# Kernel tuning notes

Hardware: AMD Instinct MI355X
Metric: run time of the kernel (lower is better)

## Reference

```python
import jax, jax.numpy as jnp
import numpy as np

B, F_DIM, H, W = 4, 256, 32, 32
DIM, DEPTH, HEADS, MLP_DIM = 768, 8, 12, 3072
DIM_HEAD = DIM // HEADS
SCALE = DIM_HEAD ** -0.5
LN_EPS = 1e-5


def sine_pos_embed(h, w, num_pos_feats):
    # PositionEmbeddingSine with normalize=True, scale=2*pi, temperature=10000
    scale = 2.0 * np.pi
    eps = 1e-6
    y = jnp.arange(1, h + 1, dtype=jnp.float32) / (h + eps) * scale  # [h]
    x = jnp.arange(1, w + 1, dtype=jnp.float32) / (w + eps) * scale  # [w]
    i = jnp.arange(num_pos_feats, dtype=jnp.float32)
    dim_t = 10000.0 ** (2.0 * jnp.floor(i / 2.0) / num_pos_feats)  # [F]

    def interleave(p):  # p: [..., F] -> sin of even dims, cos of odd dims, interleaved
        return jnp.stack([jnp.sin(p[..., 0::2]), jnp.cos(p[..., 1::2])], axis=-1).reshape(p.shape[:-1] + (-1,))

    pos_y = interleave(y[:, None] / dim_t)  # [h, F]
    pos_x = interleave(x[:, None] / dim_t)  # [w, F]
    pos = jnp.concatenate([
        jnp.broadcast_to(pos_y[:, None, :], (h, w, num_pos_feats)),
        jnp.broadcast_to(pos_x[None, :, :], (h, w, num_pos_feats)),
    ], axis=-1)  # [h, w, 2F]
    return pos.reshape(h * w, 2 * num_pos_feats)


def layer_norm(x, w, b):
    mu = jnp.mean(x, axis=-1, keepdims=True)
    var = jnp.var(x, axis=-1, keepdims=True)
    return (x - mu) * jax.lax.rsqrt(var + LN_EPS) * w + b


def setup_inputs() -> dict:
    key = jax.random.key(0)
    ks = jax.random.split(key, 16)
    s = lambda fan_in: 1.0 / np.sqrt(fan_in)
    return {
        "c_f": jax.random.normal(ks[0], (B, F_DIM, H, W), dtype=jnp.float32),
        "conv_w": jax.random.normal(ks[1], (DIM, F_DIM), dtype=jnp.float32) * s(F_DIM),
        "conv_b": jnp.zeros((DIM,), dtype=jnp.float32),
        "ln1_w": jnp.ones((DEPTH, DIM), dtype=jnp.float32),
        "ln1_b": jnp.zeros((DEPTH, DIM), dtype=jnp.float32),
        "qkv_w": jax.random.normal(ks[2], (DEPTH, DIM, 3 * DIM), dtype=jnp.float32) * s(DIM),
        "out_w": jax.random.normal(ks[3], (DEPTH, DIM, DIM), dtype=jnp.float32) * s(DIM),
        "out_b": jnp.zeros((DEPTH, DIM), dtype=jnp.float32),
        "ln2_w": jnp.ones((DEPTH, DIM), dtype=jnp.float32),
        "ln2_b": jnp.zeros((DEPTH, DIM), dtype=jnp.float32),
        "mlp_w1": jax.random.normal(ks[4], (DEPTH, DIM, MLP_DIM), dtype=jnp.float32) * s(DIM),
        "mlp_b1": jnp.zeros((DEPTH, MLP_DIM), dtype=jnp.float32),
        "mlp_w2": jax.random.normal(ks[5], (DEPTH, MLP_DIM, DIM), dtype=jnp.float32) * s(MLP_DIM),
        "mlp_b2": jnp.zeros((DEPTH, DIM), dtype=jnp.float32),
    }


def reference(c_f, conv_w, conv_b, ln1_w, ln1_b, qkv_w, out_w, out_b,
              ln2_w, ln2_b, mlp_w1, mlp_b1, mlp_w2, mlp_b2):
    b, _, h, w = c_f.shape
    n = h * w
    # 1x1 conv == per-pixel linear; tokens: [b, n, dim]
    x = jnp.einsum('bfn,df->bnd', c_f.reshape(b, F_DIM, n), conv_w) + conv_b
    x = x + sine_pos_embed(h, w, DIM // 2)[None]  # [b, n, dim]

    for l in range(DEPTH):
        # PreNorm multi-head self-attention + residual
        y = layer_norm(x, ln1_w[l], ln1_b[l])
        qkv = y @ qkv_w[l]  # [b, n, 3*dim]
        q, k, v = jnp.split(qkv, 3, axis=-1)
        to_heads = lambda t: t.reshape(b, n, HEADS, DIM_HEAD).transpose(0, 2, 1, 3)
        q, k, v = to_heads(q), to_heads(k), to_heads(v)
        dots = jnp.einsum('bhnd,bhmd->bhnm', q, k) * SCALE
        attn = jax.nn.softmax(dots, axis=-1)
        o = jnp.einsum('bhnm,bhmd->bhnd', attn, v)
        o = o.transpose(0, 2, 1, 3).reshape(b, n, DIM)
        x = o @ out_w[l] + out_b[l] + x
        # PreNorm MLP + residual
        y = layer_norm(x, ln2_w[l], ln2_b[l])
        hdd = jax.nn.gelu(y @ mlp_w1[l] + mlp_b1[l], approximate=False)
        x = hdd @ mlp_w2[l] + mlp_b2[l] + x

    return x.transpose(0, 2, 1).reshape(b, DIM, h, w)
```

## Files before the change

### kernel.cpp

```cpp
#include <hip/hip_runtime.h>
#include <stdint.h>

typedef unsigned short u16;
typedef __attribute__((ext_vector_type(8))) short short8;
typedef __attribute__((ext_vector_type(4))) short s16x4;
typedef __attribute__((ext_vector_type(4))) float f32x4;

struct P4 { float* p[4]; };

#define DEV __device__ __forceinline__

DEV u16 f2bf(float f) {
  union { float f; uint32_t u; } c; c.f = f;
  uint32_t u = c.u;
  uint32_t r = u + 0x7fffu + ((u >> 16) & 1u);
  return (u16)(r >> 16);
}

DEV void g2l16(const void* g, void* l) {
  __builtin_amdgcn_global_load_lds((__attribute__((address_space(1))) void*)(g),
                                   (__attribute__((address_space(3))) void*)(l),
                                   16, 0, 0);
}

__global__ void pos_kernel(float* __restrict__ pos) {
  int n = blockIdx.x;
  float yv = (float)((n >> 5) + 1) / (32.0f + 1e-6f) * 6.283185307179586f;
  float xv = (float)((n & 31) + 1) / (32.0f + 1e-6f) * 6.283185307179586f;
#pragma unroll
  for (int i = 0; i < 3; i++) {
    int d = threadIdx.x + i * 256;
    int dd = (d < 384) ? d : d - 384;
    float base = (d < 384) ? yv : xv;
    float ex = (float)(dd & ~1) / 384.0f;
    float arg = base / powf(10000.0f, ex);
    pos[(size_t)n * 768 + d] = (dd & 1) ? cosf(arg) : sinf(arg);
  }
}

__global__ void convw_kernel(const float* __restrict__ src, u16* __restrict__ dst) {
  int i = blockIdx.x * 256 + threadIdx.x;
  dst[i] = f2bf(src[i]);
}

DEV void tile_tr32(const float* __restrict__ src, u16* __restrict__ dst,
                   int R, int C, int tr, int tc, float (*tile)[33]) {
  int tx = threadIdx.x & 31, ty = threadIdx.x >> 5;
#pragma unroll
  for (int i = 0; i < 32; i += 8)
    tile[ty + i][tx] = src[(size_t)(tr * 32 + ty + i) * C + tc * 32 + tx];
  __syncthreads();
#pragma unroll
  for (int i = 0; i < 32; i += 8)
    dst[(size_t)(tc * 32 + ty + i) * R + tr * 32 + tx] = f2bf(tile[tx][ty + i]);
}

__global__ void wconv_kernel(const float* __restrict__ qkv_w, const float* __restrict__ out_w,
                             const float* __restrict__ m1w, const float* __restrict__ m2w,
                             u16* __restrict__ wqkv, u16* __restrict__ wout,
                             u16* __restrict__ wm1, u16* __restrict__ wm2, int layer) {
  __shared__ float tile[32][33];
  int tid = blockIdx.x;
  if (tid < 1728) {
    tile_tr32(qkv_w + (size_t)layer * 768 * 2304, wqkv, 768, 2304, tid / 72, tid % 72, tile);
  } else if (tid < 2304) {
    int t2 = tid - 1728;
    tile_tr32(out_w + (size_t)layer * 768 * 768, wout, 768, 768, t2 / 24, t2 % 24, tile);
  } else if (tid < 4608) {
    int t3 = tid - 2304;
    tile_tr32(m1w + (size_t)layer * 768 * 3072, wm1, 768, 3072, t3 / 96, t3 % 96, tile);
  } else {
    int t4 = tid - 4608;
    tile_tr32(m2w + (size_t)layer * 3072 * 768, wm2, 3072, 768, t4 / 24, t4 % 24, tile);
  }
}

__global__ void cf_tr_kernel(const float* __restrict__ c_f, u16* __restrict__ aconv) {
  __shared__ float tile[32][33];
  int b = blockIdx.z;
  tile_tr32(c_f + (size_t)b * 256 * 1024, aconv + (size_t)b * 1024 * 256,
            256, 1024, blockIdx.y, blockIdx.x, tile);
}

__global__ void out_tr_kernel(const float* __restrict__ x, float* __restrict__ out) {
  __shared__ float tile[32][33];
  int b = blockIdx.z;
  const float* src = x + (size_t)b * 1024 * 768;
  float* dst = out + (size_t)b * 768 * 1024;
  int tr = blockIdx.y, tc = blockIdx.x;
  int tx = threadIdx.x & 31, ty = threadIdx.x >> 5;
#pragma unroll
  for (int i = 0; i < 32; i += 8)
    tile[ty + i][tx] = src[(size_t)(tr * 32 + ty + i) * 768 + tc * 32 + tx];
  __syncthreads();
#pragma unroll
  for (int i = 0; i < 32; i += 8)
    dst[(size_t)(tc * 32 + ty + i) * 1024 + tr * 32 + tx] = tile[tx][ty + i];
}

__global__ __launch_bounds__(256) void ln_kernel(const float* __restrict__ x,
                                                 const float* __restrict__ w,
                                                 const float* __restrict__ bsh,
                                                 u16* __restrict__ y) {
  int row = blockIdx.x, t = threadIdx.x;
  const float* xr = x + (size_t)row * 768;
  float v[3], s = 0.f, sq = 0.f;
#pragma unroll
  for (int i = 0; i < 3; i++) { v[i] = xr[t + i * 256]; s += v[i]; sq += v[i] * v[i]; }
#pragma unroll
  for (int off = 32; off; off >>= 1) { s += __shfl_xor(s, off); sq += __shfl_xor(sq, off); }
  __shared__ float ss[4], ssq[4];
  if ((t & 63) == 0) { ss[t >> 6] = s; ssq[t >> 6] = sq; }
  __syncthreads();
  s = ss[0] + ss[1] + ss[2] + ss[3];
  sq = ssq[0] + ssq[1] + ssq[2] + ssq[3];
  float mean = s * (1.0f / 768.0f);
  float var = sq * (1.0f / 768.0f) - mean * mean;
  float rs = rsqrtf(var + 1e-5f);
#pragma unroll
  for (int i = 0; i < 3; i++) {
    int c = t + i * 256;
    y[(size_t)row * 768 + c] = f2bf((v[i] - mean) * rs * w[c] + bsh[c]);
  }
}

template <int S, bool DO_LN>
__global__ __launch_bounds__(256) void redln_kernel(P4 parts, const float* __restrict__ xin,
                                                    const float* __restrict__ bias,
                                                    const float* __restrict__ w,
                                                    const float* __restrict__ bsh,
                                                    float* __restrict__ xout,
                                                    u16* __restrict__ y) {
  int row = blockIdx.x, t = threadIdx.x;
  size_t base = (size_t)row * 768;
  float v[3], s = 0.f, sq = 0.f;
#pragma unroll
  for (int i = 0; i < 3; i++) {
    int c = t + i * 256;
    float acc = xin[base + c] + bias[c];
#pragma unroll
    for (int j = 0; j < S; j++) acc += parts.p[j][base + c];
    v[i] = acc;
    xout[base + c] = acc;
    s += acc; sq += acc * acc;
  }
  if constexpr (DO_LN) {
#pragma unroll
    for (int off = 32; off; off >>= 1) { s += __shfl_xor(s, off); sq += __shfl_xor(sq, off); }
    __shared__ float ss[4], ssq[4];
    if ((t & 63) == 0) { ss[t >> 6] = s; ssq[t >> 6] = sq; }
    __syncthreads();
    s = ss[0] + ss[1] + ss[2] + ss[3];
    sq = ssq[0] + ssq[1] + ssq[2] + ssq[3];
    float mean = s * (1.0f / 768.0f);
    float var = sq * (1.0f / 768.0f) - mean * mean;
    float rs = rsqrtf(var + 1e-5f);
#pragma unroll
    for (int i = 0; i < 3; i++) {
      int c = t + i * 256;
      y[base + c] = f2bf((v[i] - mean) * rs * w[c] + bsh[c]);
    }
  }
}

constexpr int EPI_BF16 = 0, EPI_BIAS_RES = 1, EPI_BIAS_GELU = 2, EPI_BIAS_POS = 3, EPI_PART = 4;

template <int EPI>
__global__ __launch_bounds__(256, 2) void gemm_bt(
    const u16* __restrict__ A, const u16* __restrict__ BT,
    const float* __restrict__ bias, const float* __restrict__ res,
    void* __restrict__ Cout, int M, int N, int K, P4 parts) {
  __shared__ __align__(16) u16 As[128 * 32];
  __shared__ __align__(16) u16 Bs[128 * 32];
  const int t = threadIdx.x;
  const int w = t >> 6, l = t & 63, lr = l & 15, quad = l >> 4;
  const int bm = blockIdx.y * 128, bn = blockIdx.x * 128;
  const int wm = (w & 1) * 64, wn = (w >> 1) * 64;
  f32x4 acc[4][4];
#pragma unroll
  for (int i = 0; i < 4; i++)
#pragma unroll
    for (int j = 0; j < 4; j++) acc[i][j] = (f32x4){0.f, 0.f, 0.f, 0.f};
  const int c0 = t, c1 = 256 + t;
  const size_t a0 = (size_t)(bm + (c0 >> 2)) * K + (c0 & 3) * 8;
  const size_t a1 = (size_t)(bm + (c1 >> 2)) * K + (c1 & 3) * 8;
  const size_t b0 = (size_t)(bn + (c0 >> 2)) * K + (c0 & 3) * 8;
  const size_t b1 = (size_t)(bn + (c1 >> 2)) * K + (c1 & 3) * 8;
  const int kc = K / (int)gridDim.z;
  const int kBeg = (int)blockIdx.z * kc;
  for (int k0 = kBeg; k0 < kBeg + kc; k0 += 32) {
    g2l16(A + a0 + k0, As + c0 * 8);
    g2l16(A + a1 + k0, As + c1 * 8);
    g2l16(BT + b0 + k0, Bs + c0 * 8);
    g2l16(BT + b1 + k0, Bs + c1 * 8);
    __syncthreads();
    short8 af[4], bf[4];
#pragma unroll
    for (int mi = 0; mi < 4; mi++) af[mi] = *(const short8*)(As + (wm + mi * 16 + lr) * 32 + quad * 8);
#pragma unroll
    for (int nj = 0; nj < 4; nj++) bf[nj] = *(const short8*)(Bs + (wn + nj * 16 + lr) * 32 + quad * 8);
#pragma unroll
    for (int mi = 0; mi < 4; mi++)
#pragma unroll
      for (int nj = 0; nj < 4; nj++)
        acc[mi][nj] = __builtin_amdgcn_mfma_f32_16x16x32_bf16(af[mi], bf[nj], acc[mi][nj], 0, 0, 0);
    __syncthreads();
  }
  float* Pc = (EPI == EPI_PART) ? parts.p[blockIdx.z] : nullptr;
#pragma unroll
  for (int mi = 0; mi < 4; mi++) {
    const int rowb = bm + wm + mi * 16 + quad * 4;
#pragma unroll
    for (int nj = 0; nj < 4; nj++) {
      const int gn = bn + wn + nj * 16 + lr;
#pragma unroll
      for (int r = 0; r < 4; r++) {
        const size_t idx = (size_t)(rowb + r) * N + gn;
        float v = acc[mi][nj][r];
        if constexpr (EPI == EPI_BF16) {
          ((u16*)Cout)[idx] = f2bf(v);
        } else if constexpr (EPI == EPI_BIAS_RES) {
          ((float*)Cout)[idx] = v + bias[gn] + res[idx];
        } else if constexpr (EPI == EPI_BIAS_GELU) {
          float xg = v + bias[gn];
          ((u16*)Cout)[idx] = f2bf(0.5f * xg * (1.0f + erff(xg * 0.70710678118f)));
        } else if constexpr (EPI == EPI_BIAS_POS) {
          ((float*)Cout)[idx] = v + bias[gn] + res[(size_t)((rowb + r) & 1023) * N + gn];
        } else {
          Pc[idx] = v;
        }
      }
    }
  }
}

__global__ __launch_bounds__(256) void vtr_kernel(const u16* __restrict__ qkvb,
                                                  u16* __restrict__ vT) {
  __shared__ uint32_t tile[64][65];
  const int t = threadIdx.x;
  const int bh = blockIdx.y, b = bh / 12, h = bh % 12;
  const int tok0 = blockIdx.x * 64;
  {
    int trow = t >> 2, dc = (t & 3) * 16;
    const u16* src = qkvb + (size_t)(b * 1024 + tok0 + trow) * 2304 + 1536 + h * 64 + dc;
    short8 v0 = *(const short8*)src;
    short8 v1 = *(const short8*)(src + 8);
#pragma unroll
    for (int j = 0; j < 8; j++) {
      tile[trow][dc + j] = (uint32_t)(u16)v0[j];
      tile[trow][dc + 8 + j] = (uint32_t)(u16)v1[j];
    }
  }
  __syncthreads();
  {
    int d = t >> 2, tc = (t & 3) * 16;
    short8 o0, o1;
#pragma unroll
    for (int j = 0; j < 8; j++) {
      o0[j] = (short)(u16)tile[tc + j][d];
      o1[j] = (short)(u16)tile[tc + 8 + j][d];
    }
    u16* dst = vT + (size_t)(bh * 64 + d) * 1024 + tok0 + tc;
    *(short8*)dst = o0;
    *(short8*)(dst + 8) = o1;
  }
}

__global__ __launch_bounds__(256, 3) void attn_kernel(const u16* __restrict__ qkv,
                                                      const u16* __restrict__ vT,
                                                      u16* __restrict__ o) {
  __shared__ __align__(16) u16 Ks[2][2 * 64 * 32];
  __shared__ __align__(16) u16 Vs[2][2 * 64 * 32];
  __shared__ __align__(16) u16 Ps[4][16 * 72];
  const int t = threadIdx.x;
  const int w = t >> 6, l = t & 63, lr = l & 15, quad = l >> 4;
  const int bh = blockIdx.y, b = bh / 12, h = bh % 12;
  const int qb = blockIdx.x * 64 + w * 16;
  const int swz = (lr >> 1) & 3;

  short8 aq[2];
#pragma unroll
  for (int ks = 0; ks < 2; ks++)
    aq[ks] = *(const short8*)(qkv + (size_t)(b * 1024 + qb + lr) * 2304 +
                              h * 64 + ks * 32 + quad * 8);

  const u16* kbase = qkv + (size_t)(b * 1024) * 2304 + 768 + h * 64;
  const u16* vbase = vT + (size_t)(bh * 64) * 1024;
  u16* Pw = Ps[w];

  f32x4 accO[4];
  float l_loc = 0.f;
#pragma unroll
  for (int dj = 0; dj < 4; dj++) accO[dj] = (f32x4){0.f, 0.f, 0.f, 0.f};

  auto stage = [&](int buf, int kb) {
#pragma unroll
    for (int pass = 0; pass < 2; pass++) {
      int u = pass * 256 + t;
      int ks = u >> 8, row = (u >> 2) & 63, c4 = u & 3;
      int cs = c4 ^ ((row >> 1) & 3);
      g2l16(kbase + (size_t)(kb + row) * 2304 + ks * 32 + cs * 8, Ks[buf] + (size_t)u * 8);
      g2l16(vbase + (size_t)row * 1024 + kb + ks * 32 + cs * 8, Vs[buf] + (size_t)u * 8);
    }
  };

  stage(0, 0);
  __syncthreads();
  int cur = 0;
  for (int kb = 0; kb < 1024; kb += 64) {
    if (kb + 64 < 1024) stage(cur ^ 1, kb + 64);

    f32x4 s[4];
#pragma unroll
    for (int nj = 0; nj < 4; nj++) s[nj] = (f32x4){0.f, 0.f, 0.f, 0.f};
#pragma unroll
    for (int ks = 0; ks < 2; ks++)
#pragma unroll
      for (int nj = 0; nj < 4; nj++) {
        short8 ak = *(const short8*)(Ks[cur] + ks * 2048 + (nj * 16 + lr) * 32 + (quad ^ swz) * 8);
        s[nj] = __builtin_amdgcn_mfma_f32_16x16x32_bf16(ak, aq[ks], s[nj], 0, 0, 0);
      }

    {
      const int rowoff = lr * 72;
#pragma unroll
      for (int nj = 0; nj < 4; nj++) {
        s16x4 pk;
#pragma unroll
        for (int r = 0; r < 4; r++) {
          float p = exp2f(s[nj][r] * 0.18033688011112042f);
          l_loc += p;
          pk[r] = (short)f2bf(p);
        }
        *(s16x4*)(Pw + rowoff + nj * 16 + quad * 4) = pk;
      }
    }

#pragma unroll
    for (int ks = 0; ks < 2; ks++) {
      short8 bp = *(const short8*)(Pw + lr * 72 + ks * 32 + quad * 8);
#pragma unroll
      for (int dj = 0; dj < 4; dj++) {
        short8 av = *(const short8*)(Vs[cur] + ks * 2048 + (dj * 16 + lr) * 32 + (quad ^ swz) * 8);
        accO[dj] = __builtin_amdgcn_mfma_f32_16x16x32_bf16(av, bp, accO[dj], 0, 0, 0);
      }
    }
    __syncthreads();
    cur ^= 1;
  }

  l_loc += __shfl_xor(l_loc, 16);
  l_loc += __shfl_xor(l_loc, 32);
  {
    float inv = 1.0f / l_loc;
    size_t grow = (size_t)(b * 1024 + qb + lr);
#pragma unroll
    for (int dj = 0; dj < 4; dj++) {
      s16x4 ov;
#pragma unroll
      for (int r = 0; r < 4; r++) ov[r] = (short)f2bf(accO[dj][r] * inv);
      *(s16x4*)(o + grow * 768 + h * 64 + dj * 16 + quad * 4) = ov;
    }
  }
}

extern "C" void kernel_launch(void* const* d_in, const int* in_sizes, int n_in,
                              void* d_out, int out_size, void* d_ws, size_t ws_size,
                              hipStream_t stream) {
  (void)in_sizes; (void)n_in; (void)out_size;
  const float* c_f    = (const float*)d_in[0];
  const float* conv_w = (const float*)d_in[1];
  const float* conv_b = (const float*)d_in[2];
  const float* ln1_w  = (const float*)d_in[3];
  const float* ln1_b  = (const float*)d_in[4];
  const float* qkv_w  = (const float*)d_in[5];
  const float* out_w  = (const float*)d_in[6];
  const float* out_b  = (const float*)d_in[7];
  const float* ln2_w  = (const float*)d_in[8];
  const float* ln2_b  = (const float*)d_in[9];
  const float* m1w    = (const float*)d_in[10];
  const float* m1b    = (const float*)d_in[11];
  const float* m2w    = (const float*)d_in[12];
  const float* m2b    = (const float*)d_in[13];
  float* out = (float*)d_out;

  char* p = (char*)d_ws;
  auto alloc = [&](size_t bytes) { char* q = p; p += (bytes + 255) & ~(size_t)255; return q; };
  float* pos  = (float*)alloc(1024ull * 768 * 4);
  float* x    = (float*)alloc(4096ull * 768 * 4);
  u16* y      = (u16*)alloc(4096ull * 768 * 2);
  u16* qkvb   = (u16*)alloc(4096ull * 2304 * 2);
  u16* ob     = (u16*)alloc(4096ull * 768 * 2);
  u16* hb     = (u16*)alloc(4096ull * 3072 * 2);
  u16* aconv  = (u16*)alloc(4096ull * 256 * 2);
  u16* convw  = (u16*)alloc(768ull * 256 * 2);
  u16* wqkv   = (u16*)alloc(2304ull * 768 * 2);
  u16* wout   = (u16*)alloc(768ull * 768 * 2);
  u16* wm1    = (u16*)alloc(3072ull * 768 * 2);
  u16* wm2    = (u16*)alloc(768ull * 3072 * 2);
  u16* vT = hb;

  const size_t PSZ = 4096ull * 768 * 4;
  P4 parts{};
  parts.p[0] = (float*)qkvb;
  parts.p[1] = (float*)((char*)qkvb + PSZ);
  int SPLIT = 2;
  if ((size_t)(p - (char*)d_ws) + PSZ <= ws_size) {
    parts.p[2] = (float*)out;
    parts.p[3] = (float*)alloc(PSZ);
    SPLIT = 4;
  }
  P4 none{};

  pos_kernel<<<1024, 256, 0, stream>>>(pos);
  convw_kernel<<<768, 256, 0, stream>>>(conv_w, convw);
  cf_tr_kernel<<<dim3(32, 8, 4), 256, 0, stream>>>(c_f, aconv);
  gemm_bt<EPI_BIAS_POS><<<dim3(6, 32), 256, 0, stream>>>(aconv, convw, conv_b, pos, x, 4096, 768, 256, none);

  for (int lyr = 0; lyr < 8; lyr++) {
    wconv_kernel<<<6912, 256, 0, stream>>>(qkv_w, out_w, m1w, m2w, wqkv, wout, wm1, wm2, lyr);
    if (lyr == 0) {
      ln_kernel<<<4096, 256, 0, stream>>>(x, ln1_w, ln1_b, y);
    } else if (SPLIT == 4) {
      redln_kernel<4, true><<<4096, 256, 0, stream>>>(parts, x, m2b + (lyr - 1) * 768,
                                                      ln1_w + lyr * 768, ln1_b + lyr * 768, x, y);
    } else {
      redln_kernel<2, true><<<4096, 256, 0, stream>>>(parts, x, m2b + (lyr - 1) * 768,
                                                      ln1_w + lyr * 768, ln1_b + lyr * 768, x, y);
    }
    gemm_bt<EPI_BF16><<<dim3(18, 32), 256, 0, stream>>>(y, wqkv, nullptr, nullptr, qkvb, 4096, 2304, 768, none);
    vtr_kernel<<<dim3(16, 48), 256, 0, stream>>>(qkvb, vT);
    attn_kernel<<<dim3(16, 48), 256, 0, stream>>>(qkvb, vT, ob);
    gemm_bt<EPI_BIAS_RES><<<dim3(6, 32), 256, 0, stream>>>(ob, wout, out_b + lyr * 768, x, x, 4096, 768, 768, none);
    ln_kernel<<<4096, 256, 0, stream>>>(x, ln2_w + lyr * 768, ln2_b + lyr * 768, y);
    gemm_bt<EPI_BIAS_GELU><<<dim3(24, 32), 256, 0, stream>>>(y, wm1, m1b + lyr * 3072, nullptr, hb, 4096, 3072, 768, none);
    gemm_bt<EPI_PART><<<dim3(6, 32, SPLIT), 256, 0, stream>>>(hb, wm2, nullptr, nullptr, nullptr, 4096, 768, 3072, parts);
  }
  if (SPLIT == 4) {
    redln_kernel<4, false><<<4096, 256, 0, stream>>>(parts, x, m2b + 7 * 768, nullptr, nullptr, x, nullptr);
  } else {
    redln_kernel<2, false><<<4096, 256, 0, stream>>>(parts, x, m2b + 7 * 768, nullptr, nullptr, x, nullptr);
  }
  out_tr_kernel<<<dim3(24, 32, 4), 256, 0, stream>>>(x, out);
}
```

Baseline: 1.709 ms.

## Split-K out-projection with fused reduce+LN2, always use 4-way MLP2 split

```diff
diff --git a/kernel.cpp b/kernel.cpp
--- a/kernel.cpp
+++ b/kernel.cpp
@@ -367,7 +367,7 @@
 extern "C" void kernel_launch(void* const* d_in, const int* in_sizes, int n_in,
                               void* d_out, int out_size, void* d_ws, size_t ws_size,
                               hipStream_t stream) {
-  (void)in_sizes; (void)n_in; (void)out_size;
+  (void)in_sizes; (void)n_in; (void)out_size; (void)ws_size;
   const float* c_f    = (const float*)d_in[0];
   const float* conv_w = (const float*)d_in[1];
   const float* conv_b = (const float*)d_in[2];
@@ -384,9 +384,10 @@
   const float* m2b    = (const float*)d_in[13];
   float* out = (float*)d_out;
 
+  const size_t PSZ = 4096ull * 768 * 4;
+
   char* p = (char*)d_ws;
   auto alloc = [&](size_t bytes) { char* q = p; p += (bytes + 255) & ~(size_t)255; return q; };
-  float* pos  = (float*)alloc(1024ull * 768 * 4);
   float* x    = (float*)alloc(4096ull * 768 * 4);
   u16* y      = (u16*)alloc(4096ull * 768 * 2);
   u16* qkvb   = (u16*)alloc(4096ull * 2304 * 2);
@@ -397,19 +398,18 @@
   u16* wqkv   = (u16*)alloc(2304ull * 768 * 2);
   u16* wout   = (u16*)alloc(768ull * 768 * 2);
   u16* wm1    = (u16*)alloc(3072ull * 768 * 2);
+  float* pos  = (float*)alloc(1024ull * 768 * 4);
   u16* wm2    = (u16*)alloc(768ull * 3072 * 2);
   u16* vT = hb;
 
-  const size_t PSZ = 4096ull * 768 * 4;
-  P4 parts{};
-  parts.p[0] = (float*)qkvb;
-  parts.p[1] = (float*)((char*)qkvb + PSZ);
-  int SPLIT = 2;
-  if ((size_t)(p - (char*)d_ws) + PSZ <= ws_size) {
-    parts.p[2] = (float*)out;
-    parts.p[3] = (float*)alloc(PSZ);
-    SPLIT = 4;
-  }
+  P4 pm{};
+  pm.p[0] = (float*)qkvb;
+  pm.p[1] = (float*)((char*)qkvb + PSZ);
+  pm.p[2] = (float*)out;
+  pm.p[3] = (float*)aconv;
+  P4 po{};
+  po.p[0] = (float*)qkvb;
+  po.p[1] = (float*)out;
   P4 none{};
 
   pos_kernel<<<1024, 256, 0, stream>>>(pos);
@@ -418,28 +418,22 @@
   gemm_bt<EPI_BIAS_POS><<<dim3(6, 32), 256, 0, stream>>>(aconv, convw, conv_b, pos, x, 4096, 768, 256, none);
 
   for (int lyr = 0; lyr < 8; lyr++) {
-    wconv_kernel<<<6912, 256, 0, stream>>>(qkv_w, out_w, m1w, m2w, wqkv, wout, wm1, wm2, lyr);
     if (lyr == 0) {
       ln_kernel<<<4096, 256, 0, stream>>>(x, ln1_w, ln1_b, y);
-    } else if (SPLIT == 4) {
-      redln_kernel<4, true><<<4096, 256, 0, stream>>>(parts, x, m2b + (lyr - 1) * 768,
+    } else {
+      redln_kernel<4, true><<<4096, 256, 0, stream>>>(pm, x, m2b + (lyr - 1) * 768,
                                                       ln1_w + lyr * 768, ln1_b + lyr * 768, x, y);
-    } else {
-      redln_kernel<2, true><<<4096, 256, 0, stream>>>(parts, x, m2b + (lyr - 1) * 768,
-                                                      ln1_w + lyr * 768, ln1_b + lyr * 768, x, y);
-    }
+    }
+    wconv_kernel<<<6912, 256, 0, stream>>>(qkv_w, out_w, m1w, m2w, wqkv, wout, wm1, wm2, lyr);
     gemm_bt<EPI_BF16><<<dim3(18, 32), 256, 0, stream>>>(y, wqkv, nullptr, nullptr, qkvb, 4096, 2304, 768, none);
     vtr_kernel<<<dim3(16, 48), 256, 0, stream>>>(qkvb, vT);
     attn_kernel<<<dim3(16, 48), 256, 0, stream>>>(qkvb, vT, ob);
-    gemm_bt<EPI_BIAS_RES><<<dim3(6, 32), 256, 0, stream>>>(ob, wout, out_b + lyr * 768, x, x, 4096, 768, 768, none);
-    ln_kernel<<<4096, 256, 0, stream>>>(x, ln2_w + lyr * 768, ln2_b + lyr * 768, y);
+    gemm_bt<EPI_PART><<<dim3(6, 32, 2), 256, 0, stream>>>(ob, wout, nullptr, nullptr, nullptr, 4096, 768, 768, po);
+    redln_kernel<2, true><<<4096, 256, 0, stream>>>(po, x, out_b + lyr * 768,
+                                                    ln2_w + lyr * 768, ln2_b + lyr * 768, x, y);
     gemm_bt<EPI_BIAS_GELU><<<dim3(24, 32), 256, 0, stream>>>(y, wm1, m1b + lyr * 3072, nullptr, hb, 4096, 3072, 768, none);
-    gemm_bt<EPI_PART><<<dim3(6, 32, SPLIT), 256, 0, stream>>>(hb, wm2, nullptr, nullptr, nullptr, 4096, 768, 3072, parts);
-  }
-  if (SPLIT == 4) {
-    redln_kernel<4, false><<<4096, 256, 0, stream>>>(parts, x, m2b + 7 * 768, nullptr, nullptr, x, nullptr);
-  } else {
-    redln_kernel<2, false><<<4096, 256, 0, stream>>>(parts, x, m2b + 7 * 768, nullptr, nullptr, x, nullptr);
-  }
+    gemm_bt<EPI_PART><<<dim3(6, 32, 4), 256, 0, stream>>>(hb, wm2, nullptr, nullptr, nullptr, 4096, 768, 3072, pm);
+  }
+  redln_kernel<4, false><<<4096, 256, 0, stream>>>(pm, x, m2b + 7 * 768, nullptr, nullptr, x, nullptr);
   out_tr_kernel<<<dim3(24, 32, 4), 256, 0, stream>>>(x, out);
 }
```

Result: no change. 1.688 ms (-1.2%).
